# Kernel optimization log

Hardware: AMD Instinct MI355X
Metric: run time of the kernel (lower is better)

Reference implementation:

```python
import jax, jax.numpy as jnp
import numpy as np

TEMPERATURE = 0.02
B, S, D_TOK, H = 128, 32, 128, 128  # batch, query tokens, doc tokens, hidden dim


def setup_inputs() -> dict:
    key = jax.random.key(0)
    kq, kp = jax.random.split(key)
    query_embeddings = jax.random.normal(kq, (B, S, H), dtype=jnp.float32)
    positive_embeddings = jax.random.normal(kp, (B, D_TOK, H), dtype=jnp.float32)
    return {"query_embeddings": query_embeddings, "positive_embeddings": positive_embeddings}


def reference(query_embeddings, positive_embeddings):
    # Late interaction: [b, c, s, d] = every query token vs every doc token (in-batch negatives)
    late = jnp.einsum('bsh,cdh->bcsd', query_embeddings, positive_embeddings)
    # MaxSim over doc tokens, sum over query tokens -> [b, c] score matrix
    scores = late.max(axis=-1).sum(axis=-1) / TEMPERATURE
    # In-batch negatives: label for row i is column i (the diagonal is the positive)
    logp = jax.nn.log_softmax(scores, axis=-1)
    loss = -jnp.mean(jnp.diagonal(logp))
    return loss
```

## Files before the change

kernel.cpp:

```cpp
#include <hip/hip_runtime.h>
#include <hip/hip_bf16.h>

typedef __bf16 bf16x8 __attribute__((ext_vector_type(8)));
typedef __bf16 bf16x4 __attribute__((ext_vector_type(4)));
typedef float  f32x4  __attribute__((ext_vector_type(4)));

#define P_CHUNKS (128 * 128 * 16)
#define Q_CHUNKS (128 * 32 * 16)
#define WS_NEED  ((size_t)(P_CHUNKS + Q_CHUNKS) * 16 + 128 * 128 * 4 + 4)

__global__ __launch_bounds__(256) void convert_kernel(
    const float* __restrict__ Q, const float* __restrict__ P,
    unsigned short* __restrict__ wp, unsigned short* __restrict__ wq)
{
    const int g = blockIdx.x * 256 + threadIdx.x;
    const float* src;
    unsigned short* dst;
    if (g < P_CHUNKS) {
        const int c = g >> 11, rem = g & 2047;
        const int dj = rem >> 8, k = (rem >> 6) & 3, l = rem & 63;
        src = P + ((size_t)c << 14) + (dj * 16 + (l & 15)) * 128 + k * 32 + (l >> 4) * 8;
        dst = wp + ((size_t)g << 3);
    } else {
        const int g2 = g - P_CHUNKS;
        const int b = g2 >> 9, j = g2 & 511;
        const int si = j >> 8, k = (j >> 6) & 3, l = j & 63;
        src = Q + (size_t)b * 4096 + (si * 16 + (l & 15)) * 128 + k * 32 + (l >> 4) * 8;
        dst = wq + ((size_t)g2 << 3);
    }
    float4 v0 = *(const float4*)src;
    float4 v1 = *(const float4*)(src + 4);
    bf16x8 o = { (__bf16)v0.x, (__bf16)v0.y, (__bf16)v0.z, (__bf16)v0.w,
                 (__bf16)v1.x, (__bf16)v1.y, (__bf16)v1.z, (__bf16)v1.w };
    *(bf16x8*)dst = o;
}

__global__ __launch_bounds__(256, 2) void colbert_scores_reg(
    const unsigned short* __restrict__ Pb,
    const unsigned short* __restrict__ Qb,
    float* __restrict__ scores)
{
    const int tid  = threadIdx.x;
    const int lane = tid & 63;
    const int wave = tid >> 6;

    const int xcd = blockIdx.x & 7;
    const int i   = blockIdx.x >> 3;
    const int c   = (xcd << 4) + (i & 15);
    const int qtr = i >> 4;
    const int bbase = (qtr << 5) + (wave << 3);

    const unsigned short* pw = Pb + ((size_t)c << 14);
    bf16x8 bp[8][4];
    #pragma unroll
    for (int dj = 0; dj < 8; dj++)
        #pragma unroll
        for (int k = 0; k < 4; k++)
            bp[dj][k] = *(const bf16x8*)(pw + (((dj << 2) + k) << 9) + (lane << 3));

    #pragma unroll 1
    for (int it = 0; it < 8; it++) {
        const int b = bbase + it;
        const unsigned short* qw = Qb + ((size_t)b << 12);

        bf16x8 aq[2][4];
        #pragma unroll
        for (int k = 0; k < 4; k++) {
            aq[0][k] = *(const bf16x8*)(qw + (k << 9) + (lane << 3));
            aq[1][k] = *(const bf16x8*)(qw + 2048 + (k << 9) + (lane << 3));
        }

        float mm0 = -1e30f, mm1 = -1e30f;
        #pragma unroll
        for (int dj = 0; dj < 8; dj++) {
            f32x4 t0 = (f32x4){0.f, 0.f, 0.f, 0.f};
            f32x4 t1 = (f32x4){0.f, 0.f, 0.f, 0.f};
            #pragma unroll
            for (int k = 0; k < 4; k++) {
                t0 = __builtin_amdgcn_mfma_f32_16x16x32_bf16(bp[dj][k], aq[0][k], t0, 0, 0, 0);
                t1 = __builtin_amdgcn_mfma_f32_16x16x32_bf16(bp[dj][k], aq[1][k], t1, 0, 0, 0);
            }
            #pragma unroll
            for (int r = 0; r < 4; r++) {
                mm0 = fmaxf(mm0, t0[r]);
                mm1 = fmaxf(mm1, t1[r]);
            }
        }

        mm0 = fmaxf(mm0, __shfl_xor(mm0, 16));
        mm0 = fmaxf(mm0, __shfl_xor(mm0, 32));
        mm1 = fmaxf(mm1, __shfl_xor(mm1, 16));
        mm1 = fmaxf(mm1, __shfl_xor(mm1, 32));
        float partial = mm0 + mm1;
        partial += __shfl_xor(partial, 1);
        partial += __shfl_xor(partial, 2);
        partial += __shfl_xor(partial, 4);
        partial += __shfl_xor(partial, 8);
        if (lane == 0) scores[b * 128 + c] = partial * 50.0f;
    }
}

__global__ __launch_bounds__(1024) void colbert_loss_kernel(
    const float* __restrict__ scores, unsigned* __restrict__ out)
{
    __shared__ float wpart[16];
    const int lane = threadIdx.x & 63;
    const int wave = threadIdx.x >> 6;
    float acc = 0.f;
    #pragma unroll
    for (int i = 0; i < 8; i++) {
        const int r = wave + (i << 4);
        const float* row = scores + r * 128;
        float v0 = row[lane], v1 = row[lane + 64];
        float mx = fmaxf(v0, v1);
        mx = fmaxf(mx, __shfl_xor(mx, 1));  mx = fmaxf(mx, __shfl_xor(mx, 2));
        mx = fmaxf(mx, __shfl_xor(mx, 4));  mx = fmaxf(mx, __shfl_xor(mx, 8));
        mx = fmaxf(mx, __shfl_xor(mx, 16)); mx = fmaxf(mx, __shfl_xor(mx, 32));
        float e = expf(v0 - mx) + expf(v1 - mx);
        e += __shfl_xor(e, 1);  e += __shfl_xor(e, 2);  e += __shfl_xor(e, 4);
        e += __shfl_xor(e, 8);  e += __shfl_xor(e, 16); e += __shfl_xor(e, 32);
        float diag = (r < 64) ? __shfl(v0, r) : __shfl(v1, r - 64);
        acc += diag - (mx + logf(e));
    }
    if (lane == 0) wpart[wave] = acc;
    __syncthreads();
    if (threadIdx.x == 0) {
        float t = 0.f;
        #pragma unroll
        for (int i = 0; i < 16; i++) t += wpart[i];
        float loss = -t / 128.0f;
        unsigned bits = __float_as_uint(loss);
        unsigned rnd  = (bits + 0x7FFFu + ((bits >> 16) & 1u)) & 0xFFFF0000u;
        out[0] = rnd | (rnd >> 16);
    }
}

__global__ __launch_bounds__(256, 2) void colbert_scores_slow(
    const float* __restrict__ Q, const float* __restrict__ P, float* __restrict__ scores)
{
    __shared__ __align__(16) unsigned short qs[4 * 32 * 128];
    __shared__ __align__(16) unsigned short ps[128 * 128];
    const int tid = threadIdx.x;
    const int b0 = (blockIdx.x & 31) * 4, c0 = (blockIdx.x >> 5) * 4;
    const float4* gq = (const float4*)(Q + (size_t)b0 * 4096);
    #pragma unroll
    for (int j = tid; j < 4096; j += 256) {
        float4 v = gq[j];
        int f = j << 2, row = f >> 7, h = f & 127;
        int dst = (row << 7) + (((h >> 3) ^ (row & 15)) << 3) + (h & 7);
        bf16x4 o = { (__bf16)v.x, (__bf16)v.y, (__bf16)v.z, (__bf16)v.w };
        *(bf16x4*)&qs[dst] = o;
    }
    const int lane = tid & 63, wave = tid >> 6, n = lane & 15, quad = lane >> 4;
    const unsigned short* qb = qs + wave * 4096;
    #pragma unroll 1
    for (int it = 0; it < 4; it++) {
        const int c = c0 + it;
        if (it) __syncthreads();
        const float4* gp = (const float4*)(P + (size_t)c * 16384);
        #pragma unroll
        for (int j = tid; j < 4096; j += 256) {
            float4 v = gp[j];
            int f = j << 2, d = f >> 7, h = f & 127;
            int dst = (d << 7) + (((h >> 3) ^ (d & 15)) << 3) + (h & 7);
            bf16x4 o = { (__bf16)v.x, (__bf16)v.y, (__bf16)v.z, (__bf16)v.w };
            *(bf16x4*)&ps[dst] = o;
        }
        __syncthreads();
        f32x4 acc[2][8];
        #pragma unroll
        for (int si = 0; si < 2; si++)
            #pragma unroll
            for (int dj = 0; dj < 8; dj++) acc[si][dj] = (f32x4){0.f,0.f,0.f,0.f};
        #pragma unroll
        for (int k = 0; k < 4; k++) {
            const int chunk = (((k << 2) + quad) ^ n) << 3;
            bf16x8 a0 = *(const bf16x8*)&qb[(n << 7) + chunk];
            bf16x8 a1 = *(const bf16x8*)&qb[((n + 16) << 7) + chunk];
            #pragma unroll
            for (int dj = 0; dj < 8; dj++) {
                bf16x8 bb = *(const bf16x8*)&ps[((dj * 16 + n) << 7) + chunk];
                acc[0][dj] = __builtin_amdgcn_mfma_f32_16x16x32_bf16(a0, bb, acc[0][dj], 0, 0, 0);
                acc[1][dj] = __builtin_amdgcn_mfma_f32_16x16x32_bf16(a1, bb, acc[1][dj], 0, 0, 0);
            }
        }
        float partial = 0.f;
        #pragma unroll
        for (int si = 0; si < 2; si++)
            #pragma unroll
            for (int r = 0; r < 4; r++) {
                float m = acc[si][0][r];
                #pragma unroll
                for (int dj = 1; dj < 8; dj++) m = fmaxf(m, acc[si][dj][r]);
                m = fmaxf(m, __shfl_xor(m, 1)); m = fmaxf(m, __shfl_xor(m, 2));
                m = fmaxf(m, __shfl_xor(m, 4)); m = fmaxf(m, __shfl_xor(m, 8));
                partial += m;
            }
        partial += __shfl_xor(partial, 16);
        partial += __shfl_xor(partial, 32);
        if (lane == 0) scores[(b0 + wave) * 128 + c] = partial * 50.0f;
    }
}

extern "C" void kernel_launch(void* const* d_in, const int* in_sizes, int n_in,
                              void* d_out, int out_size, void* d_ws, size_t ws_size,
                              hipStream_t stream) {
    const float* Q = (const float*)d_in[0];
    const float* P = (const float*)d_in[1];

    if (ws_size >= WS_NEED) {
        unsigned short* wp = (unsigned short*)d_ws;
        unsigned short* wq = wp + (size_t)P_CHUNKS * 8;
        float* scores = (float*)(wq + (size_t)Q_CHUNKS * 8);
        convert_kernel<<<dim3((P_CHUNKS + Q_CHUNKS) / 256), dim3(256), 0, stream>>>(
            Q, P, wp, wq);
        colbert_scores_reg<<<dim3(512), dim3(256), 0, stream>>>(wp, wq, scores);
        colbert_loss_kernel<<<dim3(1), dim3(1024), 0, stream>>>(scores, (unsigned*)d_out);
    } else {
        float* scores = (float*)d_ws;
        colbert_scores_slow<<<dim3(1024), dim3(256), 0, stream>>>(Q, P, scores);
        colbert_loss_kernel<<<dim3(1), dim3(1024), 0, stream>>>(scores, (unsigned*)d_out);
    }
}
```

Measured before the change: 86.68 us.

## Split doc tokens across wave pairs and remap convert blocks for XCD locality

The scores kernel now splits each document's 128 tokens between two waves, so each wave holds half the P fragments in registers. Partial maxima are combined through shared memory, and the grid doubles to 1024 blocks with occupancy hint 4, aiming for more parallelism and lower register pressure. The convert kernel remaps P blocks so each XCD writes the P rows that the same XCD later reads, to improve L2 locality. The cost is an added __syncthreads and LDS traffic per block.

```diff
diff --git a/kernel.cpp b/kernel.cpp
--- a/kernel.cpp
+++ b/kernel.cpp
@@ -13,16 +13,20 @@
     const float* __restrict__ Q, const float* __restrict__ P,
     unsigned short* __restrict__ wp, unsigned short* __restrict__ wq)
 {
-    const int g = blockIdx.x * 256 + threadIdx.x;
+    const int blk = blockIdx.x;
     const float* src;
     unsigned short* dst;
-    if (g < P_CHUNKS) {
-        const int c = g >> 11, rem = g & 2047;
+    if (blk < 1024) {
+        const int x   = blk & 7;
+        const int j   = blk >> 3;
+        const int c   = (x << 4) + (j & 15);
+        const int sub = j >> 4;
+        const int rem = (sub << 8) + threadIdx.x;
         const int dj = rem >> 8, k = (rem >> 6) & 3, l = rem & 63;
         src = P + ((size_t)c << 14) + (dj * 16 + (l & 15)) * 128 + k * 32 + (l >> 4) * 8;
-        dst = wp + ((size_t)g << 3);
+        dst = wp + (((size_t)(c << 11) + rem) << 3);
     } else {
-        const int g2 = g - P_CHUNKS;
+        const int g2 = (blk - 1024) * 256 + threadIdx.x;
         const int b = g2 >> 9, j = g2 & 511;
         const int si = j >> 8, k = (j >> 6) & 3, l = j & 63;
         src = Q + (size_t)b * 4096 + (si * 16 + (l & 15)) * 128 + k * 32 + (l >> 4) * 8;
@@ -35,50 +39,55 @@
     *(bf16x8*)dst = o;
 }
 
-__global__ __launch_bounds__(256, 2) void colbert_scores_reg(
+__global__ __launch_bounds__(256, 4) void colbert_scores_split(
     const unsigned short* __restrict__ Pb,
     const unsigned short* __restrict__ Qb,
     float* __restrict__ scores)
 {
+    __shared__ float smax[16][2][32];
+
     const int tid  = threadIdx.x;
     const int lane = tid & 63;
     const int wave = tid >> 6;
+    const int half = wave & 1;
+    const int pair = wave >> 1;
 
     const int xcd = blockIdx.x & 7;
-    const int i   = blockIdx.x >> 3;
-    const int c   = (xcd << 4) + (i & 15);
-    const int qtr = i >> 4;
-    const int bbase = (qtr << 5) + (wave << 3);
+    const int idx = blockIdx.x >> 3;
+    const int c   = (xcd << 4) + (idx & 15);
+    const int b0  = (idx >> 4) << 4;
 
     const unsigned short* pw = Pb + ((size_t)c << 14);
-    bf16x8 bp[8][4];
-    #pragma unroll
-    for (int dj = 0; dj < 8; dj++)
+    bf16x8 bp[4][4];
+    #pragma unroll
+    for (int dj = 0; dj < 4; dj++) {
+        const int djg = (half << 2) + dj;
         #pragma unroll
         for (int k = 0; k < 4; k++)
-            bp[dj][k] = *(const bf16x8*)(pw + (((dj << 2) + k) << 9) + (lane << 3));
+            bp[dj][k] = *(const bf16x8*)(pw + (((djg << 2) + k) << 9) + (lane << 3));
+    }
 
     #pragma unroll 1
     for (int it = 0; it < 8; it++) {
-        const int b = bbase + it;
-        const unsigned short* qw = Qb + ((size_t)b << 12);
-
-        bf16x8 aq[2][4];
+        const int bl = (pair << 3) + it;
+        const unsigned short* qw = Qb + ((size_t)(b0 + bl) << 12);
+
+        bf16x8 aq0[4], aq1[4];
         #pragma unroll
         for (int k = 0; k < 4; k++) {
-            aq[0][k] = *(const bf16x8*)(qw + (k << 9) + (lane << 3));
-            aq[1][k] = *(const bf16x8*)(qw + 2048 + (k << 9) + (lane << 3));
+            aq0[k] = *(const bf16x8*)(qw + (k << 9) + (lane << 3));
+            aq1[k] = *(const bf16x8*)(qw + 2048 + (k << 9) + (lane << 3));
         }
 
         float mm0 = -1e30f, mm1 = -1e30f;
         #pragma unroll
-        for (int dj = 0; dj < 8; dj++) {
+        for (int dj = 0; dj < 4; dj++) {
             f32x4 t0 = (f32x4){0.f, 0.f, 0.f, 0.f};
             f32x4 t1 = (f32x4){0.f, 0.f, 0.f, 0.f};
             #pragma unroll
             for (int k = 0; k < 4; k++) {
-                t0 = __builtin_amdgcn_mfma_f32_16x16x32_bf16(bp[dj][k], aq[0][k], t0, 0, 0, 0);
-                t1 = __builtin_amdgcn_mfma_f32_16x16x32_bf16(bp[dj][k], aq[1][k], t1, 0, 0, 0);
+                t0 = __builtin_amdgcn_mfma_f32_16x16x32_bf16(bp[dj][k], aq0[k], t0, 0, 0, 0);
+                t1 = __builtin_amdgcn_mfma_f32_16x16x32_bf16(bp[dj][k], aq1[k], t1, 0, 0, 0);
             }
             #pragma unroll
             for (int r = 0; r < 4; r++) {
@@ -86,17 +95,29 @@
                 mm1 = fmaxf(mm1, t1[r]);
             }
         }
-
         mm0 = fmaxf(mm0, __shfl_xor(mm0, 16));
         mm0 = fmaxf(mm0, __shfl_xor(mm0, 32));
         mm1 = fmaxf(mm1, __shfl_xor(mm1, 16));
         mm1 = fmaxf(mm1, __shfl_xor(mm1, 32));
-        float partial = mm0 + mm1;
-        partial += __shfl_xor(partial, 1);
-        partial += __shfl_xor(partial, 2);
-        partial += __shfl_xor(partial, 4);
-        partial += __shfl_xor(partial, 8);
-        if (lane == 0) scores[b * 128 + c] = partial * 50.0f;
+        if (lane < 16) {
+            smax[bl][half][lane]      = mm0;
+            smax[bl][half][16 + lane] = mm1;
+        }
+    }
+
+    __syncthreads();
+
+    #pragma unroll
+    for (int j = 0; j < 4; j++) {
+        const int bl = (wave << 2) + j;
+        const int l5 = lane & 31;
+        float v = fmaxf(smax[bl][0][l5], smax[bl][1][l5]);
+        v += __shfl_xor(v, 1);
+        v += __shfl_xor(v, 2);
+        v += __shfl_xor(v, 4);
+        v += __shfl_xor(v, 8);
+        v += __shfl_xor(v, 16);
+        if (lane == 0) scores[(b0 + bl) * 128 + c] = v * 50.0f;
     }
 }
 
@@ -212,9 +233,8 @@
         unsigned short* wp = (unsigned short*)d_ws;
         unsigned short* wq = wp + (size_t)P_CHUNKS * 8;
         float* scores = (float*)(wq + (size_t)Q_CHUNKS * 8);
-        convert_kernel<<<dim3((P_CHUNKS + Q_CHUNKS) / 256), dim3(256), 0, stream>>>(
-            Q, P, wp, wq);
-        colbert_scores_reg<<<dim3(512), dim3(256), 0, stream>>>(wp, wq, scores);
+        convert_kernel<<<dim3(1280), dim3(256), 0, stream>>>(Q, P, wp, wq);
+        colbert_scores_split<<<dim3(1024), dim3(256), 0, stream>>>(wp, wq, scores);
         colbert_loss_kernel<<<dim3(1), dim3(1024), 0, stream>>>(scores, (unsigned*)d_out);
     } else {
         float* scores = (float*)d_ws;
```

Measured after the change: 87.45 us. No clear change (+0.9%).

## Fold P bf16 conversion into scores kernel via shared-memory staging

Applied to the files above, without the earlier changes.

Drops the separate global conversion pass for the document embeddings. Each scores block now loads its fp32 P slice directly, converts it to bf16 into the MFMA fragment layout in LDS, and loads its B-fragments from there. The preprocessing kernel shrinks to a Q-only conversion. This removes the bf16 P write and re-read through global memory, but each P slice is now converted by four blocks (one per batch quarter), and a 32KB LDS buffer per block may limit occupancy.

```diff
diff --git a/kernel.cpp b/kernel.cpp
--- a/kernel.cpp
+++ b/kernel.cpp
@@ -5,41 +5,30 @@
 typedef __bf16 bf16x4 __attribute__((ext_vector_type(4)));
 typedef float  f32x4  __attribute__((ext_vector_type(4)));
 
-#define P_CHUNKS (128 * 128 * 16)
-#define Q_CHUNKS (128 * 32 * 16)
-#define WS_NEED  ((size_t)(P_CHUNKS + Q_CHUNKS) * 16 + 128 * 128 * 4 + 4)
-
-__global__ __launch_bounds__(256) void convert_kernel(
-    const float* __restrict__ Q, const float* __restrict__ P,
-    unsigned short* __restrict__ wp, unsigned short* __restrict__ wq)
+#define Q_CHUNKS (128 * 512)
+#define WS_NEED  ((size_t)Q_CHUNKS * 16 + 128 * 128 * 4)
+
+__global__ __launch_bounds__(256) void convert_q(
+    const float* __restrict__ Q, unsigned short* __restrict__ wq)
 {
     const int g = blockIdx.x * 256 + threadIdx.x;
-    const float* src;
-    unsigned short* dst;
-    if (g < P_CHUNKS) {
-        const int c = g >> 11, rem = g & 2047;
-        const int dj = rem >> 8, k = (rem >> 6) & 3, l = rem & 63;
-        src = P + ((size_t)c << 14) + (dj * 16 + (l & 15)) * 128 + k * 32 + (l >> 4) * 8;
-        dst = wp + ((size_t)g << 3);
-    } else {
-        const int g2 = g - P_CHUNKS;
-        const int b = g2 >> 9, j = g2 & 511;
-        const int si = j >> 8, k = (j >> 6) & 3, l = j & 63;
-        src = Q + (size_t)b * 4096 + (si * 16 + (l & 15)) * 128 + k * 32 + (l >> 4) * 8;
-        dst = wq + ((size_t)g2 << 3);
-    }
+    const int b = g >> 9, j = g & 511;
+    const int si = j >> 8, k = (j >> 6) & 3, l = j & 63;
+    const float* src = Q + (size_t)b * 4096 + (si * 16 + (l & 15)) * 128 + k * 32 + (l >> 4) * 8;
     float4 v0 = *(const float4*)src;
     float4 v1 = *(const float4*)(src + 4);
     bf16x8 o = { (__bf16)v0.x, (__bf16)v0.y, (__bf16)v0.z, (__bf16)v0.w,
                  (__bf16)v1.x, (__bf16)v1.y, (__bf16)v1.z, (__bf16)v1.w };
-    *(bf16x8*)dst = o;
-}
-
-__global__ __launch_bounds__(256, 2) void colbert_scores_reg(
-    const unsigned short* __restrict__ Pb,
+    *(bf16x8*)(wq + ((size_t)g << 3)) = o;
+}
+
+__global__ __launch_bounds__(256, 2) void colbert_scores_pfold(
+    const float* __restrict__ P,
     const unsigned short* __restrict__ Qb,
     float* __restrict__ scores)
 {
+    __shared__ __align__(16) unsigned short ps[128 * 128];
+
     const int tid  = threadIdx.x;
     const int lane = tid & 63;
     const int wave = tid >> 6;
@@ -50,13 +39,27 @@
     const int qtr = i >> 4;
     const int bbase = (qtr << 5) + (wave << 3);
 
-    const unsigned short* pw = Pb + ((size_t)c << 14);
+    {
+        const float4* gp = (const float4*)(P + ((size_t)c << 14));
+        #pragma unroll
+        for (int t = 0; t < 16; t++) {
+            const int j = t * 256 + tid;
+            float4 v = gp[j];
+            const int d = j >> 5, q = j & 31;
+            const int frag = ((d >> 4) << 2) + (q >> 3);
+            const int l    = (d & 15) + (((q & 7) >> 1) << 4);
+            bf16x4 o = { (__bf16)v.x, (__bf16)v.y, (__bf16)v.z, (__bf16)v.w };
+            *(bf16x4*)&ps[(frag << 9) + (l << 3) + ((q & 1) << 2)] = o;
+        }
+    }
+    __syncthreads();
+
     bf16x8 bp[8][4];
     #pragma unroll
     for (int dj = 0; dj < 8; dj++)
         #pragma unroll
         for (int k = 0; k < 4; k++)
-            bp[dj][k] = *(const bf16x8*)(pw + (((dj << 2) + k) << 9) + (lane << 3));
+            bp[dj][k] = *(const bf16x8*)&ps[(((dj << 2) + k) << 9) + (lane << 3)];
 
     #pragma unroll 1
     for (int it = 0; it < 8; it++) {
@@ -209,12 +212,10 @@
     const float* P = (const float*)d_in[1];
 
     if (ws_size >= WS_NEED) {
-        unsigned short* wp = (unsigned short*)d_ws;
-        unsigned short* wq = wp + (size_t)P_CHUNKS * 8;
+        unsigned short* wq = (unsigned short*)d_ws;
         float* scores = (float*)(wq + (size_t)Q_CHUNKS * 8);
-        convert_kernel<<<dim3((P_CHUNKS + Q_CHUNKS) / 256), dim3(256), 0, stream>>>(
-            Q, P, wp, wq);
-        colbert_scores_reg<<<dim3(512), dim3(256), 0, stream>>>(wp, wq, scores);
+        convert_q<<<dim3(256), dim3(256), 0, stream>>>(Q, wq);
+        colbert_scores_pfold<<<dim3(512), dim3(256), 0, stream>>>(P, wq, scores);
         colbert_loss_kernel<<<dim3(1), dim3(1024), 0, stream>>>(scores, (unsigned*)d_out);
     } else {
         float* scores = (float*)d_ws;
```

After: 85.50 us. About the same (-1.4%).
